# Optimization experiments

Measured on AMD Instinct MI355X. Metric: run time of the kernel, lower is better.

Reference implementation:

```python
import jax, jax.numpy as jnp
import numpy as np
from jax import lax

# Sizes
B, N, F = 8, 4096, 64          # clouds, points per cloud, feature dim
RATIO, RADIUS, K = 0.5, 0.2, 64  # fps ratio, ball radius, max_num_neighbors
S = int(N * RATIO)              # sampled centroids per cloud
H1, H2, H3 = 64, 64, 128        # MLP widths


def setup_inputs() -> dict:
    key = jax.random.key(0)
    ks = jax.random.split(key, 6)
    x = jax.random.normal(ks[0], (B * N, F), jnp.float32)
    pos = jax.random.uniform(ks[1], (B * N, 3), jnp.float32)  # unit cube
    batch = (jnp.arange(B * N) // N).astype(jnp.int32)  # equal-size clouds
    W1 = jax.random.normal(ks[2], (F + 3, H1), jnp.float32) * 0.1
    b1 = jnp.zeros((H1,), jnp.float32)
    W2 = jax.random.normal(ks[3], (H1, H2), jnp.float32) * 0.1
    b2 = jnp.zeros((H2,), jnp.float32)
    W3 = jax.random.normal(ks[4], (H2, H3), jnp.float32) * 0.1
    b3 = jnp.zeros((H3,), jnp.float32)
    return dict(x=x, pos=pos, batch=batch, W1=W1, b1=b1, W2=W2, b2=b2, W3=W3, b3=b3)


def fps_indices(pos_b):
    """Farthest point sampling for one cloud. pos_b: [N,3] -> [S] int32 indices."""
    def step(carry, _):
        cur, dmin = carry
        d = jnp.sum((pos_b - pos_b[cur]) ** 2, axis=-1)  # [N]
        dmin = jnp.minimum(dmin, d)
        nxt = jnp.argmax(dmin).astype(jnp.int32)
        return (nxt, dmin), cur
    init = (jnp.int32(0), jnp.full((N,), jnp.inf, jnp.float32))
    (_, _), sel = lax.scan(step, init, None, length=S)
    return sel


def reference(x, pos, batch, W1, b1, W2, b2, W3, b3):
    x3 = x.reshape(B, N, F)
    pos3 = pos.reshape(B, N, 3)
    batch3 = batch.reshape(B, N)

    # fps returns indices only -> no gradient path through sampling
    idx = jax.vmap(fps_indices)(lax.stop_gradient(pos3))  # [B,S]
    bi = jnp.arange(B)[:, None]
    pos_s = pos3[bi, idx]  # [B,S,3] sampled centroids

    # radius ball query: nearest-K within RADIUS (cap = max_num_neighbors)
    d2 = jnp.sum((pos_s[:, :, None, :] - pos3[:, None, :, :]) ** 2, axis=-1)  # [B,S,N]
    neg_d2, nbr = lax.top_k(-d2, K)          # [B,S,K] nearest K per centroid
    valid = (-neg_d2) <= RADIUS * RADIUS     # [B,S,K] inside-ball mask

    # PointNetConv: message = MLP(concat(x_j, pos_j - pos_i)), aggr = max
    gi = jnp.arange(B)[:, None, None]
    x_j = x3[gi, nbr]                          # [B,S,K,F]
    rel = pos3[gi, nbr] - pos_s[:, :, None, :]  # [B,S,K,3]
    h = jnp.concatenate([x_j, rel], axis=-1)    # [B,S,K,F+3]
    h = jax.nn.relu(h @ W1 + b1)
    h = jax.nn.relu(h @ W2 + b2)
    h = jax.nn.relu(h @ W3 + b3)                # [B,S,K,H3]
    h = jnp.where(valid[..., None], h, -jnp.inf)
    # each centroid is its own neighbor (dist 0 <= RADIUS), so max is finite
    out = jnp.max(h, axis=2)                    # [B,S,H3]

    x_out = out.reshape(B * S, H3)
    pos_out = pos_s.reshape(B * S, 3)
    batch_out = batch3[bi, idx].reshape(B * S)
    return x_out, pos_out, batch_out
```

## Files before the change

### kernel.cpp

```cpp
#include <hip/hip_runtime.h>
#include <cstdint>
#include <cstddef>

#define BB 8
#define NN 4096
#define FF 64
#define SS 2048
#define KK 64
#define H1c 64
#define H2c 64
#define H3c 128
#define R2 0.04f
#define CAP 448
#define NY1 240

typedef unsigned long long ull;
typedef __attribute__((ext_vector_type(4))) float f32x4;
typedef __attribute__((ext_vector_type(8))) short bf16x8;

__device__ __forceinline__ float d2_exact(float ax, float ay, float az,
                                          float bx, float by, float bz) {
  float dx = __fsub_rn(ax, bx);
  float dy = __fsub_rn(ay, by);
  float dz = __fsub_rn(az, bz);
  return __fadd_rn(__fadd_rn(__fmul_rn(dx, dx), __fmul_rn(dy, dy)), __fmul_rn(dz, dz));
}

__device__ __forceinline__ unsigned short f2bf(float f) {
  unsigned u = __float_as_uint(f);
  return (unsigned short)((u + 0x7fffu + ((u >> 16) & 1u)) >> 16);
}

#define WAVE_MAX_DPP(v)                                                        \
  do {                                                                         \
    v = max(v, __builtin_amdgcn_update_dpp(0, v, 0x111, 0xf, 0xf, true));      \
    v = max(v, __builtin_amdgcn_update_dpp(0, v, 0x112, 0xf, 0xf, true));      \
    v = max(v, __builtin_amdgcn_update_dpp(0, v, 0x114, 0xf, 0xf, true));      \
    v = max(v, __builtin_amdgcn_update_dpp(0, v, 0x118, 0xf, 0xf, true));      \
    v = max(v, __builtin_amdgcn_update_dpp(0, v, 0x142, 0xf, 0xf, true));      \
    v = max(v, __builtin_amdgcn_update_dpp(0, v, 0x143, 0xf, 0xf, true));      \
  } while (0)

__global__ __launch_bounds__(512) void fused_kernel(
    const float* __restrict__ pos, const float* __restrict__ x,
    const float* __restrict__ W1, const float* __restrict__ b1,
    const float* __restrict__ W2, const float* __restrict__ W3,
    float* __restrict__ pos_out, float* __restrict__ batch_out,
    unsigned short* __restrict__ y1b, unsigned short* __restrict__ w2p,
    unsigned short* __restrict__ w3p, float* __restrict__ xpln,
    float* __restrict__ ypln, float* __restrict__ zpln) {
  __shared__ __align__(16) char smem[49152];
  __shared__ ull skey[2][8];
  const int tid = threadIdx.x;

  if (blockIdx.x < BB) {
    float* plds = (float*)smem;
    const int b = blockIdx.x;
    const float4* src = (const float4*)(pos + (size_t)b * NN * 3);
    float4* dstl = (float4*)plds;
#pragma unroll
    for (int k = 0; k < 6; ++k) dstl[tid + k * 512] = src[tid + k * 512];
    __syncthreads();

    float px[8], py[8], pz[8], dmin[8];
#pragma unroll
    for (int i = 0; i < 8; ++i) {
      int p = tid * 8 + i;
      px[i] = plds[p * 3 + 0];
      py[i] = plds[p * 3 + 1];
      pz[i] = plds[p * 3 + 2];
      dmin[i] = INFINITY;
    }
    const int lane = tid & 63, wv = tid >> 6;
    float cx = plds[0], cy = plds[1], cz = plds[2];

    for (int s = 0; s < SS; ++s) {
      if (tid == 0) {
        int o = b * SS + s;
        pos_out[o * 3 + 0] = cx;
        pos_out[o * 3 + 1] = cy;
        pos_out[o * 3 + 2] = cz;
      }
#pragma unroll
      for (int i = 0; i < 8; ++i) {
        float d = d2_exact(px[i], py[i], pz[i], cx, cy, cz);
        dmin[i] = fminf(dmin[i], d);
      }
      float m0 = fmaxf(fmaxf(dmin[0], dmin[1]), fmaxf(dmin[2], dmin[3]));
      float m1 = fmaxf(fmaxf(dmin[4], dmin[5]), fmaxf(dmin[6], dmin[7]));
      const float lmax = fmaxf(m0, m1);
      int lidx = 0;
#pragma unroll
      for (int i = 7; i >= 0; --i)
        if (__float_as_int(dmin[i]) == __float_as_int(lmax)) lidx = i;

      const int lv = __float_as_int(lmax);
      int v = lv;
      WAVE_MAX_DPP(v);
      const int wmax = __builtin_amdgcn_readlane(v, 63);
      const ull bal = __ballot(lv == wmax);
      const int wl = (int)__builtin_ctzll(bal);
      const int wli = __builtin_amdgcn_readlane(lidx, wl);
      const int widx = ((wv << 6) + wl) * 8 + wli;
      const int buf = s & 1;
      if (lane == 0)
        skey[buf][wv] = ((ull)(unsigned)wmax << 32) | (unsigned)(~widx);
      __syncthreads();

      ull ka = skey[buf][0];
#pragma unroll
      for (int q = 1; q < 8; ++q) {
        ull kq = skey[buf][q];
        if (kq > ka) ka = kq;
      }
      const int cur = (int)(~(unsigned)(ka & 0xffffffffu));
      cx = plds[cur * 3 + 0];
      cy = plds[cur * 3 + 1];
      cz = plds[cur * 3 + 2];
    }
    for (int i = tid; i < SS; i += 512) batch_out[b * SS + i] = (float)b;
    return;
  }

  if (blockIdx.x == BB) {
    for (int e = tid; e < 4096; e += 512) {
      int j = e & 7, l = (e >> 3) & 63, s = (e >> 9) & 1, c = e >> 10;
      w2p[e] = f2bf(W2[(s * 32 + 8 * (l >> 4) + j) * H2c + c * 16 + (l & 15)]);
    }
    for (int e = tid; e < 8192; e += 512) {
      int j = e & 7, l = (e >> 3) & 63, s = (e >> 9) & 1, c = e >> 10;
      w3p[e] = f2bf(W3[(s * 32 + 8 * (l >> 4) + j) * H3c + c * 16 + (l & 15)]);
    }
    for (int i = tid; i < BB * NN; i += 512) {
      xpln[i] = pos[3 * i + 0];
      ypln[i] = pos[3 * i + 1];
      zpln[i] = pos[3 * i + 2];
    }
    return;
  }

  float(*xs)[65] = (float(*)[65])smem;
  const int cid = blockIdx.x - BB - 1;
  for (int t = cid; t < 512; t += NY1) {
    const int r0 = t * 64;
    const float4* src = (const float4*)(x + (size_t)r0 * FF);
#pragma unroll
    for (int q = 0; q < 2; q++) {
      int p = tid + q * 512;
      float4 v = src[p];
      int row = (p * 4) >> 6, col = (p * 4) & 63;
      xs[row][col + 0] = v.x;
      xs[row][col + 1] = v.y;
      xs[row][col + 2] = v.z;
      xs[row][col + 3] = v.w;
    }
    __syncthreads();
    const int c4 = (tid & 15) * 4, kb = (tid >> 4) * 2;
    float acc[2][4];
#pragma unroll
    for (int kq = 0; kq < 2; kq++) {
      acc[kq][0] = b1[c4 + 0];
      acc[kq][1] = b1[c4 + 1];
      acc[kq][2] = b1[c4 + 2];
      acc[kq][3] = b1[c4 + 3];
    }
    for (int f = 0; f < FF; ++f) {
      float4 w = *(const float4*)(W1 + f * H1c + c4);
#pragma unroll
      for (int kq = 0; kq < 2; kq++) {
        float a = xs[kb + kq][f];
        acc[kq][0] += a * w.x;
        acc[kq][1] += a * w.y;
        acc[kq][2] += a * w.z;
        acc[kq][3] += a * w.w;
      }
    }
#pragma unroll
    for (int kq = 0; kq < 2; kq++) {
      ushort4 o;
      o.x = f2bf(acc[kq][0]);
      o.y = f2bf(acc[kq][1]);
      o.z = f2bf(acc[kq][2]);
      o.w = f2bf(acc[kq][3]);
      *(ushort4*)(y1b + (size_t)(r0 + kb + kq) * H1c + c4) = o;
    }
    __syncthreads();
  }
}

__global__ __launch_bounds__(256) void bqmlp_kernel(
    const float* __restrict__ pos, const float* __restrict__ xpln,
    const float* __restrict__ ypln, const float* __restrict__ zpln,
    const unsigned short* __restrict__ y1b, const float* __restrict__ W1,
    const float* __restrict__ b2, const float* __restrict__ b3,
    const unsigned short* __restrict__ w2p, const unsigned short* __restrict__ w3p,
    const float* __restrict__ pos_out, float* __restrict__ x_out) {
  __shared__ __align__(16) unsigned short lw2[4096];
  __shared__ __align__(16) unsigned short lw3[8192];
  __shared__ float w1r[3][64];
  __shared__ __align__(16) ull kc[4][CAP];
  __shared__ int nbl[4][64];
  __shared__ float red[4][128];
  __shared__ __align__(16) unsigned short h2t[4][16][88];
  const int tid = threadIdx.x;
  const int lane = tid & 63, wv = tid >> 6;
  const int lrow = lane & 15, g16 = lane >> 4;

  {
    const uint4* s2 = (const uint4*)w2p;
    uint4* d2v = (uint4*)lw2;
    for (int i = tid; i < 512; i += 256) d2v[i] = s2[i];
    const uint4* s3 = (const uint4*)w3p;
    uint4* d3v = (uint4*)lw3;
    for (int i = tid; i < 1024; i += 256) d3v[i] = s3[i];
    if (tid < 192) w1r[tid / 64][tid % 64] = W1[(64 + tid / 64) * H1c + (tid % 64)];
  }
  const bf16x8* w2f = (const bf16x8*)lw2;
  const bf16x8* w3f = (const bf16x8*)lw3;

  const int g0 = blockIdx.x * 4;
  const int b = blockIdx.x >> 9;
  const float4* xp4 = (const float4*)(xpln + (size_t)b * NN);
  const float4* yp4 = (const float4*)(ypln + (size_t)b * NN);
  const float4* zp4 = (const float4*)(zpln + (size_t)b * NN);

  {
    const int g = g0 + wv;
    const float cx = pos_out[g * 3 + 0], cy = pos_out[g * 3 + 1],
                cz = pos_out[g * 3 + 2];
    const ull lt = (1ull << lane) - 1ull;
    int cnt = 0;
    for (int t = 0; t < 16; ++t) {
      const int f4 = t * 64 + lane;
      float4 xv = xp4[f4], yv = yp4[f4], zv = zp4[f4];
      const int j0 = f4 * 4;
      {
        float d2 = d2_exact(xv.x, yv.x, zv.x, cx, cy, cz);
        bool pred = (d2 <= R2);
        ull mask = __ballot(pred);
        if (pred) {
          int p = cnt + (int)__popcll(mask & lt);
          if (p < CAP) kc[wv][p] = ((ull)__float_as_uint(d2) << 32) | (unsigned)(j0 + 0);
        }
        cnt += (int)__popcll(mask);
      }
      {
        float d2 = d2_exact(xv.y, yv.y, zv.y, cx, cy, cz);
        bool pred = (d2 <= R2);
        ull mask = __ballot(pred);
        if (pred) {
          int p = cnt + (int)__popcll(mask & lt);
          if (p < CAP) kc[wv][p] = ((ull)__float_as_uint(d2) << 32) | (unsigned)(j0 + 1);
        }
        cnt += (int)__popcll(mask);
      }
      {
        float d2 = d2_exact(xv.z, yv.z, zv.z, cx, cy, cz);
        bool pred = (d2 <= R2);
        ull mask = __ballot(pred);
        if (pred) {
          int p = cnt + (int)__popcll(mask & lt);
          if (p < CAP) kc[wv][p] = ((ull)__float_as_uint(d2) << 32) | (unsigned)(j0 + 2);
        }
        cnt += (int)__popcll(mask);
      }
      {
        float d2 = d2_exact(xv.w, yv.w, zv.w, cx, cy, cz);
        bool pred = (d2 <= R2);
        ull mask = __ballot(pred);
        if (pred) {
          int p = cnt + (int)__popcll(mask & lt);
          if (p < CAP) kc[wv][p] = ((ull)__float_as_uint(d2) << 32) | (unsigned)(j0 + 3);
        }
        cnt += (int)__popcll(mask);
      }
    }
    int M = cnt < CAP ? cnt : CAP;

    if (M <= 64) {
      nbl[wv][lane] =
          (lane < M) ? (b * NN + (int)(unsigned)(kc[wv][lane] & 0xffffffffu)) : -1;
    } else {
      ull mk[7];
      int rk[7];
#pragma unroll
      for (int q = 0; q < 7; q++) {
        int p = lane + q * 64;
        mk[q] = (p < M) ? kc[wv][p] : ~0ull;
        rk[q] = 0;
      }
      int i = 0;
      for (; i + 2 <= M; i += 2) {
        ull ka = kc[wv][i], kb2 = kc[wv][i + 1];
#pragma unroll
        for (int q = 0; q < 7; q++)
          rk[q] += (int)(ka < mk[q]) + (int)(kb2 < mk[q]);
      }
      if (i < M) {
        ull ka = kc[wv][i];
#pragma unroll
        for (int q = 0; q < 7; q++) rk[q] += (int)(ka < mk[q]);
      }
#pragma unroll
      for (int q = 0; q < 7; q++) {
        int p = lane + q * 64;
        if (p < M && rk[q] < KK)
          nbl[wv][rk[q]] = b * NN + (int)(unsigned)(mk[q] & 0xffffffffu);
      }
    }
  }
  __syncthreads();

  for (int pass = 0; pass < 4; ++pass) {
    const int g = g0 + pass;
    const float cx = pos_out[g * 3 + 0], cy = pos_out[g * 3 + 1],
                cz = pos_out[g * 3 + 2];
    const int* nl = nbl[pass];

    const int r = wv * 16 + lrow;
    const int j = nl[r];

    bf16x8 a0 = (bf16x8)0, a1 = (bf16x8)0;
    if (j >= 0) {
      const float rx = pos[j * 3 + 0] - cx;
      const float ry = pos[j * 3 + 1] - cy;
      const float rz = pos[j * 3 + 2] - cz;
      const unsigned short* yr = y1b + (size_t)j * H1c;
      uint4 vlo = *(const uint4*)(yr + 8 * g16);
      uint4 vhi = *(const uint4*)(yr + 32 + 8 * g16);
      const unsigned* plo = (const unsigned*)&vlo;
      const unsigned* phi = (const unsigned*)&vhi;
#pragma unroll
      for (int q = 0; q < 4; ++q) {
        unsigned u = plo[q];
        int k0 = 8 * g16 + 2 * q;
        float e0 = __uint_as_float(u << 16) + rx * w1r[0][k0] + ry * w1r[1][k0] +
                   rz * w1r[2][k0];
        float e1 = __uint_as_float(u & 0xffff0000u) + rx * w1r[0][k0 + 1] +
                   ry * w1r[1][k0 + 1] + rz * w1r[2][k0 + 1];
        a0[2 * q] = (short)f2bf(fmaxf(e0, 0.f));
        a0[2 * q + 1] = (short)f2bf(fmaxf(e1, 0.f));
        unsigned u2 = phi[q];
        int k1 = 32 + k0;
        float f0 = __uint_as_float(u2 << 16) + rx * w1r[0][k1] + ry * w1r[1][k1] +
                   rz * w1r[2][k1];
        float f1 = __uint_as_float(u2 & 0xffff0000u) + rx * w1r[0][k1 + 1] +
                   ry * w1r[1][k1 + 1] + rz * w1r[2][k1 + 1];
        a1[2 * q] = (short)f2bf(fmaxf(f0, 0.f));
        a1[2 * q + 1] = (short)f2bf(fmaxf(f1, 0.f));
      }
    }

#pragma unroll
    for (int c = 0; c < 4; ++c) {
      float bb = b2[c * 16 + lrow];
      f32x4 acc = {bb, bb, bb, bb};
      acc = __builtin_amdgcn_mfma_f32_16x16x32_bf16(a0, w2f[(c * 2 + 0) * 64 + lane], acc, 0, 0, 0);
      acc = __builtin_amdgcn_mfma_f32_16x16x32_bf16(a1, w2f[(c * 2 + 1) * 64 + lane], acc, 0, 0, 0);
#pragma unroll
      for (int t = 0; t < 4; ++t)
        h2t[wv][4 * g16 + t][c * 16 + lrow] = f2bf(fmaxf(acc[t], 0.f));
    }

    bf16x8 a20 = *(const bf16x8*)&h2t[wv][lrow][8 * g16];
    bf16x8 a21 = *(const bf16x8*)&h2t[wv][lrow][32 + 8 * g16];

    float vmax[8];
#pragma unroll
    for (int c = 0; c < 8; ++c) {
      float bb = b3[c * 16 + lrow];
      f32x4 acc = {bb, bb, bb, bb};
      acc = __builtin_amdgcn_mfma_f32_16x16x32_bf16(a20, w3f[(c * 2 + 0) * 64 + lane], acc, 0, 0, 0);
      acc = __builtin_amdgcn_mfma_f32_16x16x32_bf16(a21, w3f[(c * 2 + 1) * 64 + lane], acc, 0, 0, 0);
      float m = -INFINITY;
#pragma unroll
      for (int t = 0; t < 4; ++t) {
        int rg = wv * 16 + 4 * g16 + t;
        float val = (nl[rg] >= 0) ? fmaxf(acc[t], 0.f) : -INFINITY;
        m = fmaxf(m, val);
      }
      m = fmaxf(m, __shfl_xor(m, 16));
      m = fmaxf(m, __shfl_xor(m, 32));
      vmax[c] = m;
    }
    if (g16 == 0) {
#pragma unroll
      for (int c = 0; c < 8; ++c) red[wv][c * 16 + lrow] = vmax[c];
    }
    __syncthreads();
    if (tid < H3c) {
      float m = fmaxf(fmaxf(red[0][tid], red[1][tid]), fmaxf(red[2][tid], red[3][tid]));
      x_out[(size_t)g * H3c + tid] = m;
    }
    __syncthreads();
  }
}

extern "C" void kernel_launch(void* const* d_in, const int* in_sizes, int n_in,
                              void* d_out, int out_size, void* d_ws, size_t ws_size,
                              hipStream_t stream) {
  const float* x = (const float*)d_in[0];
  const float* pos = (const float*)d_in[1];
  const float* W1 = (const float*)d_in[3];
  const float* b1 = (const float*)d_in[4];
  const float* W2 = (const float*)d_in[5];
  const float* b2 = (const float*)d_in[6];
  const float* W3 = (const float*)d_in[7];
  const float* b3 = (const float*)d_in[8];

  float* out = (float*)d_out;
  float* x_out = out;
  float* pos_out = out + (size_t)BB * SS * H3c;
  float* batch_out = pos_out + (size_t)BB * SS * 3;

  const size_t y1_bytes = (size_t)BB * NN * H1c * sizeof(unsigned short);
  const size_t w2p_bytes = 4096 * sizeof(unsigned short);
  const size_t w3p_bytes = 8192 * sizeof(unsigned short);
  const size_t pln_bytes = (size_t)BB * NN * sizeof(float);
  if (ws_size < y1_bytes + w2p_bytes + w3p_bytes + 3 * pln_bytes) return;
  unsigned short* y1b = (unsigned short*)d_ws;
  unsigned short* w2p = (unsigned short*)((char*)d_ws + y1_bytes);
  unsigned short* w3p = w2p + 4096;
  float* xpln = (float*)((char*)d_ws + y1_bytes + w2p_bytes + w3p_bytes);
  float* ypln = xpln + BB * NN;
  float* zpln = ypln + BB * NN;

  fused_kernel<<<BB + 1 + NY1, 512, 0, stream>>>(pos, x, W1, b1, W2, W3, pos_out,
                                                 batch_out, y1b, w2p, w3p, xpln,
                                                 ypln, zpln);
  bqmlp_kernel<<<BB * SS / 4, 256, 0, stream>>>(pos, xpln, ypln, zpln, y1b, W1,
                                                b2, b3, w2p, w3p, pos_out, x_out);
}
```

Before: 1.352 ms.

## Fuse ball-query MLP into persistent kernel overlapping FPS via chunk flags

```diff
diff --git a/kernel.cpp b/kernel.cpp
--- a/kernel.cpp
+++ b/kernel.cpp
@@ -11,7 +11,8 @@
 #define H2c 64
 #define H3c 128
 #define R2 0.04f
-#define CAP 448
+#define CAPQ 304
+#define QRANK 5
 #define NY1 240
 
 typedef unsigned long long ull;
@@ -45,13 +46,21 @@
     const float* __restrict__ pos, const float* __restrict__ x,
     const float* __restrict__ W1, const float* __restrict__ b1,
     const float* __restrict__ W2, const float* __restrict__ W3,
+    const float* __restrict__ b2, const float* __restrict__ b3,
     float* __restrict__ pos_out, float* __restrict__ batch_out,
     unsigned short* __restrict__ y1b, unsigned short* __restrict__ w2p,
     unsigned short* __restrict__ w3p, float* __restrict__ xpln,
-    float* __restrict__ ypln, float* __restrict__ zpln) {
-  __shared__ __align__(16) char smem[49152];
+    float* __restrict__ ypln, float* __restrict__ zpln,
+    float* __restrict__ posw, int* __restrict__ flags, int* __restrict__ ycnt,
+    float* __restrict__ x_out) {
+  __shared__ __align__(16) char smem[49408];
   __shared__ ull skey[2][8];
+  __shared__ float xs[64][65];
+  __shared__ __align__(16) unsigned short lw2[4096];
+  __shared__ __align__(16) unsigned short lw3[8192];
+  __shared__ float w1r[3][64];
   const int tid = threadIdx.x;
+  const int lane = tid & 63, wv = tid >> 6;
 
   if (blockIdx.x < BB) {
     float* plds = (float*)smem;
@@ -71,7 +80,6 @@
       pz[i] = plds[p * 3 + 2];
       dmin[i] = INFINITY;
     }
-    const int lane = tid & 63, wv = tid >> 6;
     float cx = plds[0], cy = plds[1], cz = plds[2];
 
     for (int s = 0; s < SS; ++s) {
@@ -80,6 +88,17 @@
         pos_out[o * 3 + 0] = cx;
         pos_out[o * 3 + 1] = cy;
         pos_out[o * 3 + 2] = cz;
+        __hip_atomic_store(&posw[o * 3 + 0], cx, __ATOMIC_RELAXED,
+                           __HIP_MEMORY_SCOPE_AGENT);
+        __hip_atomic_store(&posw[o * 3 + 1], cy, __ATOMIC_RELAXED,
+                           __HIP_MEMORY_SCOPE_AGENT);
+        __hip_atomic_store(&posw[o * 3 + 2], cz, __ATOMIC_RELAXED,
+                           __HIP_MEMORY_SCOPE_AGENT);
+        if ((s & 255) == 255) {
+          asm volatile("s_waitcnt vmcnt(0)" ::: "memory");
+          __hip_atomic_store(&flags[b * 8 + (s >> 8)], 1, __ATOMIC_RELAXED,
+                             __HIP_MEMORY_SCOPE_AGENT);
+        }
       }
 #pragma unroll
       for (int i = 0; i < 8; ++i) {
@@ -136,11 +155,14 @@
       ypln[i] = pos[3 * i + 1];
       zpln[i] = pos[3 * i + 2];
     }
+    __syncthreads();
+    if (tid == 0)
+      __hip_atomic_fetch_add(ycnt, 1, __ATOMIC_RELEASE, __HIP_MEMORY_SCOPE_AGENT);
     return;
   }
 
-  float(*xs)[65] = (float(*)[65])smem;
   const int cid = blockIdx.x - BB - 1;
+
   for (int t = cid; t < 512; t += NY1) {
     const int r0 = t * 64;
     const float4* src = (const float4*)(x + (size_t)r0 * FF);
@@ -186,213 +208,209 @@
     }
     __syncthreads();
   }
-}
-
-__global__ __launch_bounds__(256) void bqmlp_kernel(
-    const float* __restrict__ pos, const float* __restrict__ xpln,
-    const float* __restrict__ ypln, const float* __restrict__ zpln,
-    const unsigned short* __restrict__ y1b, const float* __restrict__ W1,
-    const float* __restrict__ b2, const float* __restrict__ b3,
-    const unsigned short* __restrict__ w2p, const unsigned short* __restrict__ w3p,
-    const float* __restrict__ pos_out, float* __restrict__ x_out) {
-  __shared__ __align__(16) unsigned short lw2[4096];
-  __shared__ __align__(16) unsigned short lw3[8192];
-  __shared__ float w1r[3][64];
-  __shared__ __align__(16) ull kc[4][CAP];
-  __shared__ int nbl[4][64];
-  __shared__ float red[4][128];
-  __shared__ __align__(16) unsigned short h2t[4][16][88];
-  const int tid = threadIdx.x;
-  const int lane = tid & 63, wv = tid >> 6;
-  const int lrow = lane & 15, g16 = lane >> 4;
+  if (tid == 0)
+    __hip_atomic_fetch_add(ycnt, 1, __ATOMIC_RELEASE, __HIP_MEMORY_SCOPE_AGENT);
+
+  while (__hip_atomic_load(ycnt, __ATOMIC_RELAXED, __HIP_MEMORY_SCOPE_AGENT) <
+         NY1 + 1)
+    __builtin_amdgcn_s_sleep(32);
+  if (lane == 0)
+    (void)__hip_atomic_load(ycnt, __ATOMIC_ACQUIRE, __HIP_MEMORY_SCOPE_AGENT);
+  __syncthreads();
 
   {
     const uint4* s2 = (const uint4*)w2p;
     uint4* d2v = (uint4*)lw2;
-    for (int i = tid; i < 512; i += 256) d2v[i] = s2[i];
+    for (int i = tid; i < 512; i += 512) d2v[i] = s2[i];
     const uint4* s3 = (const uint4*)w3p;
     uint4* d3v = (uint4*)lw3;
-    for (int i = tid; i < 1024; i += 256) d3v[i] = s3[i];
+    for (int i = tid; i < 1024; i += 512) d3v[i] = s3[i];
     if (tid < 192) w1r[tid / 64][tid % 64] = W1[(64 + tid / 64) * H1c + (tid % 64)];
   }
+  __syncthreads();
   const bf16x8* w2f = (const bf16x8*)lw2;
   const bf16x8* w3f = (const bf16x8*)lw3;
 
-  const int g0 = blockIdx.x * 4;
-  const int b = blockIdx.x >> 9;
-  const float4* xp4 = (const float4*)(xpln + (size_t)b * NN);
-  const float4* yp4 = (const float4*)(ypln + (size_t)b * NN);
-  const float4* zp4 = (const float4*)(zpln + (size_t)b * NN);
-
-  {
-    const int g = g0 + wv;
-    const float cx = pos_out[g * 3 + 0], cy = pos_out[g * 3 + 1],
-                cz = pos_out[g * 3 + 2];
-    const ull lt = (1ull << lane) - 1ull;
-    int cnt = 0;
-    for (int t = 0; t < 16; ++t) {
-      const int f4 = t * 64 + lane;
-      float4 xv = xp4[f4], yv = yp4[f4], zv = zp4[f4];
-      const int j0 = f4 * 4;
-      {
-        float d2 = d2_exact(xv.x, yv.x, zv.x, cx, cy, cz);
-        bool pred = (d2 <= R2);
-        ull mask = __ballot(pred);
-        if (pred) {
-          int p = cnt + (int)__popcll(mask & lt);
-          if (p < CAP) kc[wv][p] = ((ull)__float_as_uint(d2) << 32) | (unsigned)(j0 + 0);
-        }
-        cnt += (int)__popcll(mask);
-      }
-      {
-        float d2 = d2_exact(xv.y, yv.y, zv.y, cx, cy, cz);
-        bool pred = (d2 <= R2);
-        ull mask = __ballot(pred);
-        if (pred) {
-          int p = cnt + (int)__popcll(mask & lt);
-          if (p < CAP) kc[wv][p] = ((ull)__float_as_uint(d2) << 32) | (unsigned)(j0 + 1);
-        }
-        cnt += (int)__popcll(mask);
-      }
-      {
-        float d2 = d2_exact(xv.z, yv.z, zv.z, cx, cy, cz);
-        bool pred = (d2 <= R2);
-        ull mask = __ballot(pred);
-        if (pred) {
-          int p = cnt + (int)__popcll(mask & lt);
-          if (p < CAP) kc[wv][p] = ((ull)__float_as_uint(d2) << 32) | (unsigned)(j0 + 2);
-        }
-        cnt += (int)__popcll(mask);
-      }
-      {
-        float d2 = d2_exact(xv.w, yv.w, zv.w, cx, cy, cz);
-        bool pred = (d2 <= R2);
-        ull mask = __ballot(pred);
-        if (pred) {
-          int p = cnt + (int)__popcll(mask & lt);
-          if (p < CAP) kc[wv][p] = ((ull)__float_as_uint(d2) << 32) | (unsigned)(j0 + 3);
-        }
-        cnt += (int)__popcll(mask);
-      }
-    }
-    int M = cnt < CAP ? cnt : CAP;
-
-    if (M <= 64) {
-      nbl[wv][lane] =
-          (lane < M) ? (b * NN + (int)(unsigned)(kc[wv][lane] & 0xffffffffu)) : -1;
-    } else {
-      ull mk[7];
-      int rk[7];
-#pragma unroll
-      for (int q = 0; q < 7; q++) {
-        int p = lane + q * 64;
-        mk[q] = (p < M) ? kc[wv][p] : ~0ull;
-        rk[q] = 0;
-      }
-      int i = 0;
-      for (; i + 2 <= M; i += 2) {
-        ull ka = kc[wv][i], kb2 = kc[wv][i + 1];
-#pragma unroll
-        for (int q = 0; q < 7; q++)
-          rk[q] += (int)(ka < mk[q]) + (int)(kb2 < mk[q]);
-      }
-      if (i < M) {
-        ull ka = kc[wv][i];
-#pragma unroll
-        for (int q = 0; q < 7; q++) rk[q] += (int)(ka < mk[q]);
-      }
-#pragma unroll
-      for (int q = 0; q < 7; q++) {
-        int p = lane + q * 64;
-        if (p < M && rk[q] < KK)
-          nbl[wv][rk[q]] = b * NN + (int)(unsigned)(mk[q] & 0xffffffffu);
-      }
-    }
-  }
-  __syncthreads();
-
-  for (int pass = 0; pass < 4; ++pass) {
-    const int g = g0 + pass;
-    const float cx = pos_out[g * 3 + 0], cy = pos_out[g * 3 + 1],
-                cz = pos_out[g * 3 + 2];
-    const int* nl = nbl[pass];
-
-    const int r = wv * 16 + lrow;
-    const int j = nl[r];
-
-    bf16x8 a0 = (bf16x8)0, a1 = (bf16x8)0;
-    if (j >= 0) {
-      const float rx = pos[j * 3 + 0] - cx;
-      const float ry = pos[j * 3 + 1] - cy;
-      const float rz = pos[j * 3 + 2] - cz;
-      const unsigned short* yr = y1b + (size_t)j * H1c;
-      uint4 vlo = *(const uint4*)(yr + 8 * g16);
-      uint4 vhi = *(const uint4*)(yr + 32 + 8 * g16);
-      const unsigned* plo = (const unsigned*)&vlo;
-      const unsigned* phi = (const unsigned*)&vhi;
-#pragma unroll
-      for (int q = 0; q < 4; ++q) {
-        unsigned u = plo[q];
-        int k0 = 8 * g16 + 2 * q;
-        float e0 = __uint_as_float(u << 16) + rx * w1r[0][k0] + ry * w1r[1][k0] +
-                   rz * w1r[2][k0];
-        float e1 = __uint_as_float(u & 0xffff0000u) + rx * w1r[0][k0 + 1] +
-                   ry * w1r[1][k0 + 1] + rz * w1r[2][k0 + 1];
-        a0[2 * q] = (short)f2bf(fmaxf(e0, 0.f));
-        a0[2 * q + 1] = (short)f2bf(fmaxf(e1, 0.f));
-        unsigned u2 = phi[q];
-        int k1 = 32 + k0;
-        float f0 = __uint_as_float(u2 << 16) + rx * w1r[0][k1] + ry * w1r[1][k1] +
-                   rz * w1r[2][k1];
-        float f1 = __uint_as_float(u2 & 0xffff0000u) + rx * w1r[0][k1 + 1] +
-                   ry * w1r[1][k1 + 1] + rz * w1r[2][k1 + 1];
-        a1[2 * q] = (short)f2bf(fmaxf(f0, 0.f));
-        a1[2 * q + 1] = (short)f2bf(fmaxf(f1, 0.f));
-      }
-    }
-
-#pragma unroll
-    for (int c = 0; c < 4; ++c) {
-      float bb = b2[c * 16 + lrow];
-      f32x4 acc = {bb, bb, bb, bb};
-      acc = __builtin_amdgcn_mfma_f32_16x16x32_bf16(a0, w2f[(c * 2 + 0) * 64 + lane], acc, 0, 0, 0);
-      acc = __builtin_amdgcn_mfma_f32_16x16x32_bf16(a1, w2f[(c * 2 + 1) * 64 + lane], acc, 0, 0, 0);
-#pragma unroll
-      for (int t = 0; t < 4; ++t)
-        h2t[wv][4 * g16 + t][c * 16 + lrow] = f2bf(fmaxf(acc[t], 0.f));
-    }
-
-    bf16x8 a20 = *(const bf16x8*)&h2t[wv][lrow][8 * g16];
-    bf16x8 a21 = *(const bf16x8*)&h2t[wv][lrow][32 + 8 * g16];
-
-    float vmax[8];
-#pragma unroll
-    for (int c = 0; c < 8; ++c) {
-      float bb = b3[c * 16 + lrow];
-      f32x4 acc = {bb, bb, bb, bb};
-      acc = __builtin_amdgcn_mfma_f32_16x16x32_bf16(a20, w3f[(c * 2 + 0) * 64 + lane], acc, 0, 0, 0);
-      acc = __builtin_amdgcn_mfma_f32_16x16x32_bf16(a21, w3f[(c * 2 + 1) * 64 + lane], acc, 0, 0, 0);
-      float m = -INFINITY;
-#pragma unroll
-      for (int t = 0; t < 4; ++t) {
-        int rg = wv * 16 + 4 * g16 + t;
-        float val = (nl[rg] >= 0) ? fmaxf(acc[t], 0.f) : -INFINITY;
-        m = fmaxf(m, val);
-      }
-      m = fmaxf(m, __shfl_xor(m, 16));
-      m = fmaxf(m, __shfl_xor(m, 32));
-      vmax[c] = m;
-    }
-    if (g16 == 0) {
-#pragma unroll
-      for (int c = 0; c < 8; ++c) red[wv][c * 16 + lrow] = vmax[c];
+  ull(*kc)[CAPQ] = (ull(*)[CAPQ])(smem);
+  unsigned short(*h2t)[16][88] = (unsigned short(*)[16][88])(smem + 19456);
+  float(*red)[128] = (float(*)[128])(smem + 41984);
+  int(*nbl)[64] = (int(*)[64])(smem + 46080);
+  float(*cc)[4] = (float(*)[4])(smem + 48128);
+
+  const int lrow = lane & 15, g16 = lane >> 4;
+
+  for (int it = cid; it < 2048; it += NY1) {
+    const int k = it >> 8;
+    const int rr = it & 255;
+    const int b = rr >> 5;
+    const int j32 = rr & 31;
+    const int g0 = b * SS + k * 256 + j32 * 8;
+
+    while (__hip_atomic_load(&flags[b * 8 + k], __ATOMIC_RELAXED,
+                             __HIP_MEMORY_SCOPE_AGENT) == 0)
+      __builtin_amdgcn_s_sleep(32);
+    asm volatile("" ::: "memory");
+
+    {
+      const int g = g0 + wv;
+      const float cx = __hip_atomic_load(&posw[g * 3 + 0], __ATOMIC_RELAXED,
+                                         __HIP_MEMORY_SCOPE_AGENT);
+      const float cy = __hip_atomic_load(&posw[g * 3 + 1], __ATOMIC_RELAXED,
+                                         __HIP_MEMORY_SCOPE_AGENT);
+      const float cz = __hip_atomic_load(&posw[g * 3 + 2], __ATOMIC_RELAXED,
+                                         __HIP_MEMORY_SCOPE_AGENT);
+      if (lane == 0) {
+        cc[wv][0] = cx;
+        cc[wv][1] = cy;
+        cc[wv][2] = cz;
+      }
+      const float4* xp4 = (const float4*)(xpln + (size_t)b * NN);
+      const float4* yp4 = (const float4*)(ypln + (size_t)b * NN);
+      const float4* zp4 = (const float4*)(zpln + (size_t)b * NN);
+      const ull lt = (1ull << lane) - 1ull;
+      int cnt = 0;
+      for (int t = 0; t < 16; ++t) {
+        const int f4 = t * 64 + lane;
+        float4 xv = xp4[f4], yv = yp4[f4], zv = zp4[f4];
+        const int j0 = f4 * 4;
+        float dd[4];
+        dd[0] = d2_exact(xv.x, yv.x, zv.x, cx, cy, cz);
+        dd[1] = d2_exact(xv.y, yv.y, zv.y, cx, cy, cz);
+        dd[2] = d2_exact(xv.z, yv.z, zv.z, cx, cy, cz);
+        dd[3] = d2_exact(xv.w, yv.w, zv.w, cx, cy, cz);
+#pragma unroll
+        for (int e = 0; e < 4; ++e) {
+          bool pred = (dd[e] <= R2);
+          ull mask = __ballot(pred);
+          if (pred) {
+            int p = cnt + (int)__popcll(mask & lt);
+            if (p < CAPQ)
+              kc[wv][p] = ((ull)__float_as_uint(dd[e]) << 32) | (unsigned)(j0 + e);
+          }
+          cnt += (int)__popcll(mask);
+        }
+      }
+      int M = cnt < CAPQ ? cnt : CAPQ;
+
+      if (M <= 64) {
+        nbl[wv][lane] =
+            (lane < M) ? (b * NN + (int)(unsigned)(kc[wv][lane] & 0xffffffffu)) : -1;
+      } else {
+        ull mk[QRANK];
+        int rk[QRANK];
+#pragma unroll
+        for (int q = 0; q < QRANK; q++) {
+          int p = lane + q * 64;
+          mk[q] = (p < M) ? kc[wv][p] : ~0ull;
+          rk[q] = 0;
+        }
+        int i = 0;
+        for (; i + 2 <= M; i += 2) {
+          ull ka = kc[wv][i], kb2 = kc[wv][i + 1];
+#pragma unroll
+          for (int q = 0; q < QRANK; q++)
+            rk[q] += (int)(ka < mk[q]) + (int)(kb2 < mk[q]);
+        }
+        if (i < M) {
+          ull ka = kc[wv][i];
+#pragma unroll
+          for (int q = 0; q < QRANK; q++) rk[q] += (int)(ka < mk[q]);
+        }
+#pragma unroll
+        for (int q = 0; q < QRANK; q++) {
+          int p = lane + q * 64;
+          if (p < M && rk[q] < KK)
+            nbl[wv][rk[q]] = b * NN + (int)(unsigned)(mk[q] & 0xffffffffu);
+        }
+      }
     }
     __syncthreads();
-    if (tid < H3c) {
-      float m = fmaxf(fmaxf(red[0][tid], red[1][tid]), fmaxf(red[2][tid], red[3][tid]));
-      x_out[(size_t)g * H3c + tid] = m;
-    }
-    __syncthreads();
+
+    const int grp = wv >> 2, lw = wv & 3;
+    for (int p = 0; p < 4; ++p) {
+      const int ci = p * 2 + grp;
+      const int* nl = nbl[ci];
+      const float cx = cc[ci][0], cy = cc[ci][1], cz = cc[ci][2];
+      const int r = lw * 16 + lrow;
+      const int j = nl[r];
+
+      bf16x8 a0 = (bf16x8)0, a1 = (bf16x8)0;
+      if (j >= 0) {
+        const float rx = pos[j * 3 + 0] - cx;
+        const float ry = pos[j * 3 + 1] - cy;
+        const float rz = pos[j * 3 + 2] - cz;
+        const unsigned short* yr = y1b + (size_t)j * H1c;
+        uint4 vlo = *(const uint4*)(yr + 8 * g16);
+        uint4 vhi = *(const uint4*)(yr + 32 + 8 * g16);
+        const unsigned* plo = (const unsigned*)&vlo;
+        const unsigned* phi = (const unsigned*)&vhi;
+#pragma unroll
+        for (int q = 0; q < 4; ++q) {
+          unsigned u = plo[q];
+          int k0 = 8 * g16 + 2 * q;
+          float e0 = __uint_as_float(u << 16) + rx * w1r[0][k0] + ry * w1r[1][k0] +
+                     rz * w1r[2][k0];
+          float e1 = __uint_as_float(u & 0xffff0000u) + rx * w1r[0][k0 + 1] +
+                     ry * w1r[1][k0 + 1] + rz * w1r[2][k0 + 1];
+          a0[2 * q] = (short)f2bf(fmaxf(e0, 0.f));
+          a0[2 * q + 1] = (short)f2bf(fmaxf(e1, 0.f));
+          unsigned u2 = phi[q];
+          int k1 = 32 + k0;
+          float f0 = __uint_as_float(u2 << 16) + rx * w1r[0][k1] + ry * w1r[1][k1] +
+                     rz * w1r[2][k1];
+          float f1 = __uint_as_float(u2 & 0xffff0000u) + rx * w1r[0][k1 + 1] +
+                     ry * w1r[1][k1 + 1] + rz * w1r[2][k1 + 1];
+          a1[2 * q] = (short)f2bf(fmaxf(f0, 0.f));
+          a1[2 * q + 1] = (short)f2bf(fmaxf(f1, 0.f));
+        }
+      }
+
+#pragma unroll
+      for (int c = 0; c < 4; ++c) {
+        float bb = b2[c * 16 + lrow];
+        f32x4 acc = {bb, bb, bb, bb};
+        acc = __builtin_amdgcn_mfma_f32_16x16x32_bf16(a0, w2f[(c * 2 + 0) * 64 + lane], acc, 0, 0, 0);
+        acc = __builtin_amdgcn_mfma_f32_16x16x32_bf16(a1, w2f[(c * 2 + 1) * 64 + lane], acc, 0, 0, 0);
+#pragma unroll
+        for (int t = 0; t < 4; ++t)
+          h2t[wv][4 * g16 + t][c * 16 + lrow] = f2bf(fmaxf(acc[t], 0.f));
+      }
+
+      bf16x8 a20 = *(const bf16x8*)&h2t[wv][lrow][8 * g16];
+      bf16x8 a21 = *(const bf16x8*)&h2t[wv][lrow][32 + 8 * g16];
+
+      float vmax[8];
+#pragma unroll
+      for (int c = 0; c < 8; ++c) {
+        float bb = b3[c * 16 + lrow];
+        f32x4 acc = {bb, bb, bb, bb};
+        acc = __builtin_amdgcn_mfma_f32_16x16x32_bf16(a20, w3f[(c * 2 + 0) * 64 + lane], acc, 0, 0, 0);
+        acc = __builtin_amdgcn_mfma_f32_16x16x32_bf16(a21, w3f[(c * 2 + 1) * 64 + lane], acc, 0, 0, 0);
+        float m = -INFINITY;
+#pragma unroll
+        for (int t = 0; t < 4; ++t) {
+          int rg = lw * 16 + 4 * g16 + t;
+          float val = (nl[rg] >= 0) ? fmaxf(acc[t], 0.f) : -INFINITY;
+          m = fmaxf(m, val);
+        }
+        m = fmaxf(m, __shfl_xor(m, 16));
+        m = fmaxf(m, __shfl_xor(m, 32));
+        vmax[c] = m;
+      }
+      if (g16 == 0) {
+#pragma unroll
+        for (int c = 0; c < 8; ++c) red[wv][c * 16 + lrow] = vmax[c];
+      }
+      __syncthreads();
+      if (tid < 256) {
+        const int which = tid >> 7, col = tid & 127;
+        const float* rb = red[which * 4];
+        float m = fmaxf(fmaxf(rb[col], rb[128 + col]),
+                        fmaxf(rb[256 + col], rb[384 + col]));
+        x_out[(size_t)(g0 + p * 2 + which) * H3c + col] = m;
+      }
+      __syncthreads();
+    }
   }
 }
 
@@ -417,17 +435,23 @@
   const size_t w2p_bytes = 4096 * sizeof(unsigned short);
   const size_t w3p_bytes = 8192 * sizeof(unsigned short);
   const size_t pln_bytes = (size_t)BB * NN * sizeof(float);
-  if (ws_size < y1_bytes + w2p_bytes + w3p_bytes + 3 * pln_bytes) return;
-  unsigned short* y1b = (unsigned short*)d_ws;
-  unsigned short* w2p = (unsigned short*)((char*)d_ws + y1_bytes);
-  unsigned short* w3p = w2p + 4096;
-  float* xpln = (float*)((char*)d_ws + y1_bytes + w2p_bytes + w3p_bytes);
-  float* ypln = xpln + BB * NN;
-  float* zpln = ypln + BB * NN;
-
-  fused_kernel<<<BB + 1 + NY1, 512, 0, stream>>>(pos, x, W1, b1, W2, W3, pos_out,
-                                                 batch_out, y1b, w2p, w3p, xpln,
-                                                 ypln, zpln);
-  bqmlp_kernel<<<BB * SS / 4, 256, 0, stream>>>(pos, xpln, ypln, zpln, y1b, W1,
-                                                b2, b3, w2p, w3p, pos_out, x_out);
+  const size_t posw_bytes = (size_t)BB * SS * 3 * sizeof(float);
+  const size_t need =
+      y1_bytes + w2p_bytes + w3p_bytes + 3 * pln_bytes + posw_bytes + 512;
+  if (ws_size < need) return;
+  char* p = (char*)d_ws;
+  unsigned short* y1b = (unsigned short*)p;            p += y1_bytes;
+  unsigned short* w2p = (unsigned short*)p;            p += w2p_bytes;
+  unsigned short* w3p = (unsigned short*)p;            p += w3p_bytes;
+  float* xpln = (float*)p;                             p += pln_bytes;
+  float* ypln = (float*)p;                             p += pln_bytes;
+  float* zpln = (float*)p;                             p += pln_bytes;
+  float* posw = (float*)p;                             p += posw_bytes;
+  int* flags = (int*)p;
+  int* ycnt = flags + 64;
+
+  hipMemsetAsync(flags, 0, 512, stream);
+  fused_kernel<<<BB + 1 + NY1, 512, 0, stream>>>(
+      pos, x, W1, b1, W2, W3, b2, b3, pos_out, batch_out, y1b, w2p, w3p, xpln,
+      ypln, zpln, posw, flags, ycnt, x_out);
 }
```

After: 1.228 ms. -9.2%, faster.
